# Kernel tuning notes

Measured on AMD Instinct MI355X. Metric: run time of the kernel, lower is better.

The kernel has to match this reference:

```python
import jax, jax.numpy as jnp
import numpy as np

B, T, I, H, O = 256, 128, 64, 2048, 24


def setup_inputs() -> dict:
    key = jax.random.key(0)
    ks = jax.random.split(key, 10)
    sI = 1.0 / np.sqrt(I)
    sH = 1.0 / np.sqrt(H)
    return {
        "trains": jax.random.normal(ks[0], (B, T, I), jnp.float32),
        "dec": jax.random.normal(ks[1], (B, O - 1), jnp.float32),
        # packed gate projections, order [i, f, o, c] along last dim
        "Wx": jax.random.normal(ks[2], (I, 4 * H), jnp.float32) * sI,
        "bx": jax.random.normal(ks[3], (4 * H,), jnp.float32) * sI,
        "Wh": jax.random.normal(ks[4], (H, 4 * H), jnp.float32) * sH,
        "bh": jax.random.normal(ks[5], (4 * H,), jnp.float32) * sH,
        "Win": jax.random.normal(ks[6], (1, I), jnp.float32),
        "b_in": jax.random.normal(ks[7], (I,), jnp.float32),
        "Wout": jax.random.normal(ks[8], (H, 1), jnp.float32) * sH,
        "bout": jax.random.normal(ks[9], (1,), jnp.float32) * sH,
    }


def reference(trains, dec, Wx, bx, Wh, bh, Win, b_in, Wout, bout):
    def cell(h, c, x):
        # fused gate GEMMs: x@Wx and h@Wh each produce all 4 gates at once
        g = x @ Wx + bx + h @ Wh + bh  # [B, 4H]
        i, f, o, cc = jnp.split(g, 4, axis=-1)
        c = jax.nn.sigmoid(f) * c + jax.nn.sigmoid(i) * jnp.tanh(cc)
        h = jax.nn.sigmoid(o) * jnp.tanh(c)
        return h, c

    b = trains.shape[0]
    hdim = Wh.shape[0]
    h0 = jnp.zeros((b, hdim), trains.dtype)
    c0 = jnp.zeros((b, hdim), trains.dtype)

    def enc_step(carry, x):
        h, c = cell(*carry, x)
        return (h, c), None

    (h, c), _ = jax.lax.scan(enc_step, (h0, c0), jnp.swapaxes(trains, 0, 1))
    y1 = h @ Wout + bout  # [B, 1]

    def dec_step(carry, x_scalar):
        x = x_scalar[:, None] @ Win + b_in  # [B, I]
        h, c = cell(*carry, x)
        return (h, c), h @ Wout + bout  # emit [B, 1]

    (h, c), ys = jax.lax.scan(dec_step, (h, c), dec.T)  # ys: [O-1, B, 1]
    return jnp.concatenate([y1, jnp.swapaxes(ys[..., 0], 0, 1)], axis=1)  # [B, O]
```

## Files before the change

### kernel.cpp

```cpp
#include <hip/hip_runtime.h>


#define NB 256
#define NH 2048
#define NI 64
#define NK 2112
#define NPK 8192
#define NSTEPS 151
#define NO 24

typedef int i32x4 __attribute__((ext_vector_type(4)));
typedef int i32x16 __attribute__((ext_vector_type(16)));
typedef float f32x4 __attribute__((ext_vector_type(4)));
typedef unsigned short u16;
typedef unsigned char u8;
typedef unsigned long long u64;

__device__ __forceinline__ void gload16(const void* g, void* l) {
  __builtin_amdgcn_global_load_lds(
      (const __attribute__((address_space(1))) unsigned int*)g,
      (__attribute__((address_space(3))) unsigned int*)l, 16, 0, 0);
}

__device__ __forceinline__ int q8(float v) {
  int q = __float2int_rn(v);
  return q > 127 ? 127 : (q < -127 ? -127 : q);
}

__device__ __forceinline__ float sigmoidf_(float x) { return 1.f / (1.f + __expf(-x)); }
__device__ __forceinline__ float tanhf_(float x) {
  x = fminf(15.f, fmaxf(-15.f, x));
  float e = __expf(2.f * x);
  return (e - 1.f) / (e + 1.f);
}

__global__ __launch_bounds__(256) void wl_colmax(const float* __restrict__ Wx,
                                                 const float* __restrict__ Wh,
                                                 float* __restrict__ sp,
                                                 float* __restrict__ rq) {
  __shared__ float red[4][64];
  const int jl = threadIdx.x & 63, ks = threadIdx.x >> 6;
  const int j = blockIdx.x * 64 + jl;
  float m = 0.f;
  for (int k = ks * 528; k < ks * 528 + 528; ++k) {
    float v = (k < NH) ? Wh[(size_t)k * NPK + j] : Wx[(size_t)(k - NH) * NPK + j];
    m = fmaxf(m, fabsf(v));
  }
  red[ks][jl] = m;
  __syncthreads();
  if (ks == 0) {
    m = fmaxf(fmaxf(red[0][jl], red[1][jl]), fmaxf(red[2][jl], red[3][jl]));
    int p = (j & (NH - 1)) * 4 + (j >> 11);
    sp[p] = m * (1.f / 127.f);
    rq[p] = (m > 0.f) ? 127.f / m : 0.f;
  }
}

__global__ __launch_bounds__(256) void wl_pack_w(const float* __restrict__ Wx,
                                                 const float* __restrict__ Wh,
                                                 const float* __restrict__ rq,
                                                 u8* __restrict__ Wq) {
  __shared__ float s[64][65];
  const int j0 = blockIdx.x * 64, k0 = blockIdx.y * 64;
  const int jl = threadIdx.x & 63, kg = threadIdx.x >> 6;
#pragma unroll
  for (int it = 0; it < 16; ++it) {
    int kl = it * 4 + kg;
    int k = k0 + kl, j = j0 + jl;
    float v = (k < NH) ? Wh[(size_t)k * NPK + j] : Wx[(size_t)(k - NH) * NPK + j];
    s[kl][jl] = v;
  }
  __syncthreads();
  const int j = j0 + jl;
  const int p = (j & (NH - 1)) * 4 + (j >> 11);
  const int cs = p >> 6, col = p & 63;
  const float r = rq[p];
  union { u8 b[16]; i32x4 v; } q;
#pragma unroll
  for (int e = 0; e < 16; ++e) q.b[e] = (u8)(signed char)q8(s[kg * 16 + e][jl] * r);
  *(i32x4*)(Wq + ((size_t)(cs * 33 + blockIdx.y) * 4 + kg) * 1024 + col * 16) = q.v;
}

__global__ __launch_bounds__(256) void wl_bsum(const float* __restrict__ bx,
                                               const float* __restrict__ bh,
                                               float* __restrict__ bsum) {
  int p = blockIdx.x * 256 + threadIdx.x;
  int j = (p & 3) * NH + (p >> 2);
  bsum[p] = bx[j] + bh[j];
}

__global__ __launch_bounds__(256) void wl_xall(const float* __restrict__ trains,
                                               const float* __restrict__ dec,
                                               const float* __restrict__ Win,
                                               const float* __restrict__ b_in,
                                               u8* __restrict__ xfH,
                                               u8* __restrict__ xfL,
                                               float* __restrict__ sx) {
  const int t = blockIdx.x, b = threadIdx.x;
  float x[64];
  if (t < 128) {
    const float4* src = (const float4*)(trains + ((size_t)b * 128 + t) * 64);
#pragma unroll
    for (int i = 0; i < 16; ++i) {
      float4 v = src[i];
      x[4 * i] = v.x; x[4 * i + 1] = v.y; x[4 * i + 2] = v.z; x[4 * i + 3] = v.w;
    }
  } else {
    float d = dec[b * 23 + (t - 128)];
#pragma unroll
    for (int i = 0; i < 64; ++i) x[i] = d * Win[i] + b_in[i];
  }
  float m = 0.f;
#pragma unroll
  for (int i = 0; i < 64; ++i) m = fmaxf(m, fabsf(x[i]));
  float sv, r;
  if (m > 1e-30f) { sv = m * (1.f / 127.f); r = 127.f / m; }
  else            { sv = 1.f; r = 0.f; }
  sx[t * 256 + b] = sv;
  const size_t base = (size_t)t * 16384 + (b >> 5) * 2048;
#pragma unroll
  for (int kc = 0; kc < 2; ++kc)
#pragma unroll
    for (int lhh = 0; lhh < 2; ++lhh) {
      union { u8 b16[16]; i32x4 v; } wh, wl;
#pragma unroll
      for (int e = 0; e < 16; ++e) {
        float xs = x[kc * 32 + lhh * 16 + e] * r;
        int hi = q8(xs);
        int lo = q8((xs - (float)hi) * 254.f);
        wh.b16[e] = (u8)(signed char)hi;
        wl.b16[e] = (u8)(signed char)lo;
      }
      size_t off = base + kc * 1024 + (lhh * 32 + (b & 31)) * 16;
      *(i32x4*)(xfH + off) = wh.v;
      *(i32x4*)(xfL + off) = wl.v;
    }
}

__global__ __launch_bounds__(256, 1) void wl_step(const u8* __restrict__ Wq,
                                                  const float* __restrict__ bsum,
                                                  const float* __restrict__ sp,
                                                  const u8* __restrict__ xfH,
                                                  const u8* __restrict__ xfL,
                                                  const float* __restrict__ sx,
                                                  u8* __restrict__ hfH,
                                                  u8* __restrict__ hfL,
                                                  float* __restrict__ c_t,
                                                  float* __restrict__ ypart,
                                                  const float* __restrict__ Wout,
                                                  int t) {
  __shared__ char arena[90112];

  const int bid = blockIdx.x;
  const int cs = (bid & 7) * 16 + ((bid >> 3) & 15);
  const int rh = bid >> 7;
  const int p0 = cs * 64, u0 = cs * 16, b0 = rh * 128;

  const int tid = threadIdx.x;
  const int wv = tid >> 6, lane = tid & 63;
  const int l31 = lane & 31, lh = lane >> 5;

  const int par = t & 1;
  const u8* __restrict__ hinH = hfH + (size_t)par * 524288;
  const u8* __restrict__ hinL = hfL + (size_t)par * 524288;
  u8* __restrict__ houtH = hfH + (size_t)(par ^ 1) * 524288;
  u8* __restrict__ houtL = hfL + (size_t)(par ^ 1) * 524288;

  const int rb = rh * 4 + wv;
  const size_t aoff = (size_t)rb * 65536 + lane * 16;
  const size_t xoff = (size_t)t * 16384 + rb * 2048 + lane * 16;
  const u8* const wsrc = Wq + (size_t)cs * 135168 + wv * 1024 + lane * 16;

  i32x16 aH0h = {}, aH0l = {}, aH1h = {}, aH1l = {};
  i32x16 aX0h = {}, aX0l = {}, aX1h = {}, aX1l = {};
  i32x4 A[4][4];

  auto stageB = [&](int kt, int buf) {
    gload16(wsrc + (size_t)kt * 4096, arena + buf * 4096 + wv * 1024);
  };
  auto loadA = [&](int kt, int slot) {
    if (kt < 32) {
      A[slot][0] = *(const i32x4*)(hinH + aoff + (size_t)(2 * kt) * 1024);
      A[slot][1] = *(const i32x4*)(hinH + aoff + (size_t)(2 * kt + 1) * 1024);
      A[slot][2] = *(const i32x4*)(hinL + aoff + (size_t)(2 * kt) * 1024);
      A[slot][3] = *(const i32x4*)(hinL + aoff + (size_t)(2 * kt + 1) * 1024);
    } else {
      A[slot][0] = *(const i32x4*)(xfH + xoff);
      A[slot][1] = *(const i32x4*)(xfH + xoff + 1024);
      A[slot][2] = *(const i32x4*)(xfL + xoff);
      A[slot][3] = *(const i32x4*)(xfL + xoff + 1024);
    }
  };
  auto compute = [&](int kt, int buf) {
    const char* Bb = arena + buf * 4096;
    const int slot = kt & 3;
#pragma unroll
    for (int kh = 0; kh < 2; ++kh) {
      i32x4 b0 = *(const i32x4*)(Bb + (kh * 2 + lh) * 1024 + l31 * 16);
      i32x4 b1 = *(const i32x4*)(Bb + (kh * 2 + lh) * 1024 + (32 + l31) * 16);
      i32x4 ah = A[slot][kh], al = A[slot][2 + kh];
      if (kt < 32) {
        aH0h = __builtin_amdgcn_mfma_i32_32x32x32_i8(ah, b0, aH0h, 0, 0, 0);
        aH1h = __builtin_amdgcn_mfma_i32_32x32x32_i8(ah, b1, aH1h, 0, 0, 0);
        aH0l = __builtin_amdgcn_mfma_i32_32x32x32_i8(al, b0, aH0l, 0, 0, 0);
        aH1l = __builtin_amdgcn_mfma_i32_32x32x32_i8(al, b1, aH1l, 0, 0, 0);
      } else {
        aX0h = __builtin_amdgcn_mfma_i32_32x32x32_i8(ah, b0, aX0h, 0, 0, 0);
        aX1h = __builtin_amdgcn_mfma_i32_32x32x32_i8(ah, b1, aX1h, 0, 0, 0);
        aX0l = __builtin_amdgcn_mfma_i32_32x32x32_i8(al, b0, aX0l, 0, 0, 0);
        aX1l = __builtin_amdgcn_mfma_i32_32x32x32_i8(al, b1, aX1l, 0, 0, 0);
      }
    }
  };

  stageB(0, 0); stageB(1, 1); stageB(2, 2); stageB(3, 3);
  loadA(0, 0); loadA(1, 1); loadA(2, 2);
#pragma unroll
  for (int kt = 0; kt < 33; ++kt) {
    if (kt + 4 <= 32) stageB(kt + 4, (kt + 4) % 6);
    if (kt + 3 <= 32) loadA(kt + 3, (kt + 3) & 3);
    if (kt == 0)       asm volatile("s_waitcnt vmcnt(13)" ::: "memory");
    else if (kt == 1)  asm volatile("s_waitcnt vmcnt(14)" ::: "memory");
    else if (kt <= 28) asm volatile("s_waitcnt vmcnt(15)" ::: "memory");
    else if (kt == 29) asm volatile("s_waitcnt vmcnt(14)" ::: "memory");
    else if (kt == 30) asm volatile("s_waitcnt vmcnt(9)" ::: "memory");
    else if (kt == 31) asm volatile("s_waitcnt vmcnt(4)" ::: "memory");
    else               asm volatile("s_waitcnt vmcnt(0)" ::: "memory");
    asm volatile("s_barrier" ::: "memory");
    compute(kt, kt % 6);
  }

  {
    char* const gH = arena + 24576;
    char* const gX = arena + 57344;
    const float s0 = sp[p0 + l31], s1 = sp[p0 + 32 + l31];
#pragma unroll
    for (int cb = 0; cb < 2; ++cb) {
      const i32x16& ahh = cb ? aH1h : aH0h;
      const i32x16& ahl = cb ? aH1l : aH0l;
      const i32x16& axh = cb ? aX1h : aX0h;
      const i32x16& axl = cb ? aX1l : aX0l;
      const float spc = cb ? s1 : s0;
      const float fH = spc * (1.f / 127.f);
      const int col = cb * 32 + l31;
#pragma unroll
      for (int q = 0; q < 4; ++q) {
        f32x4 vH, vX;
#pragma unroll
        for (int e = 0; e < 4; ++e) {
          vH[e] = fH * ((float)ahh[4 * q + e] + (float)ahl[4 * q + e] * (1.f / 254.f));
          vX[e] = spc * ((float)axh[4 * q + e] + (float)axl[4 * q + e] * (1.f / 254.f));
        }
        int chunk = wv * 8 + q * 2 + lh;
        *(f32x4*)(gH + col * 512 + ((chunk ^ (col & 7)) << 4)) = vH;
        *(f32x4*)(gX + col * 512 + ((chunk ^ (col & 7)) << 4)) = vX;
      }
    }
  }
  __syncthreads();

  {
    const char* const gH = arena + 24576;
    const char* const gX = arena + 57344;
    const int bl = tid & 127, ug = tid >> 7;
    const int bg = b0 + bl;
    const float sxv = sx[t * 256 + bg];
    const bool emit = (t >= 127);
    float yacc = 0.f;
    union { u8 q[8]; u64 v; } hqh, hql;
#pragma unroll
    for (int j = 0; j < 8; ++j) {
      int ul = ug * 8 + j;
      float g[4];
#pragma unroll
      for (int gi = 0; gi < 4; ++gi) {
        int col = ul * 4 + gi;
        int off = col * 512 + (((bl >> 2) ^ (col & 7)) << 4) + (bl & 3) * 4;
        g[gi] = *(const float*)(gH + off) + sxv * *(const float*)(gX + off);
      }
      const float4 bs = *(const float4*)(bsum + p0 + ul * 4);
      float si = sigmoidf_(g[0] + bs.x);
      float sf = sigmoidf_(g[1] + bs.y);
      float so = sigmoidf_(g[2] + bs.z);
      float tc = tanhf_(g[3] + bs.w);
      size_t ci = (size_t)(u0 + ul) * NB + bg;
      float cn = sf * c_t[ci] + si * tc;
      float h = so * tanhf_(cn);
      c_t[ci] = cn;
      float hs = h * 127.f;
      int hi = q8(hs);
      int lo = q8((hs - (float)hi) * 254.f);
      hqh.q[j] = (u8)(signed char)hi;
      hql.q[j] = (u8)(signed char)lo;
      if (emit) yacc += h * Wout[u0 + ul];
    }
    size_t hoff = ((size_t)((bg >> 5) * 64 + (cs >> 1)) * 64 +
                   (cs & 1) * 32 + (bg & 31)) * 16 + ug * 8;
    *(u64*)(houtH + hoff) = hqh.v;
    *(u64*)(houtL + hoff) = hql.v;
    if (emit) ypart[((size_t)(t - 127) * 256 + cs * 2 + ug) * NB + bg] = yacc;
  }
}

__global__ __launch_bounds__(256) void wl_finy(const float* __restrict__ ypart,
                                               const float* __restrict__ bout,
                                               float* __restrict__ out) {
  int j = blockIdx.x;
  int b = threadIdx.x;
  const float* yp = ypart + (size_t)j * 256 * NB;
  float s = bout[0];
#pragma unroll 8
  for (int i = 0; i < 256; ++i) s += yp[i * NB + b];
  out[b * NO + j] = s;
}

extern "C" void kernel_launch(void* const* d_in, const int* in_sizes, int n_in,
                              void* d_out, int out_size, void* d_ws, size_t ws_size,
                              hipStream_t stream) {
  const float* trains = (const float*)d_in[0];
  const float* dec    = (const float*)d_in[1];
  const float* Wx     = (const float*)d_in[2];
  const float* bx     = (const float*)d_in[3];
  const float* Wh     = (const float*)d_in[4];
  const float* bh     = (const float*)d_in[5];
  const float* Win    = (const float*)d_in[6];
  const float* b_in   = (const float*)d_in[7];
  const float* Wout   = (const float*)d_in[8];
  const float* bout   = (const float*)d_in[9];
  float* out = (float*)d_out;
  char* ws = (char*)d_ws;

  u8*    Wq    = (u8*)(ws);
  float* sp    = (float*)(ws + 17301504);
  float* rq    = (float*)(ws + 17334272);
  float* bsum  = (float*)(ws + 17367040);
  u8*    xfH   = (u8*)(ws + 17399808);
  u8*    xfL   = (u8*)(ws + 19873792);
  float* sx    = (float*)(ws + 22347776);
  u8*    hfH   = (u8*)(ws + 23550976);
  u8*    hfL   = (u8*)(ws + 24599552);
  float* c_t   = (float*)(ws + 25648128);
  float* ypart = (float*)(ws + 27745280);

  (void)hipMemsetAsync(ws + 23550976, 0, 4194304, stream);
  wl_colmax<<<128, 256, 0, stream>>>(Wx, Wh, sp, rq);
  wl_pack_w<<<dim3(128, 33), 256, 0, stream>>>(Wx, Wh, rq, Wq);
  wl_bsum<<<32, 256, 0, stream>>>(bx, bh, bsum);
  wl_xall<<<NSTEPS, 256, 0, stream>>>(trains, dec, Win, b_in, xfH, xfL, sx);
  for (int t = 0; t < NSTEPS; ++t)
    wl_step<<<256, 256, 0, stream>>>(Wq, bsum, sp, xfH, xfL, sx, hfH, hfL,
                                     c_t, ypart, Wout, t);
  wl_finy<<<NO, 256, 0, stream>>>(ypart, bout, out);
}
```

Before: 2.447 ms.

## Retile LSTM step to 128x64 tiles with LDS-staged A and split colmax

The per-step kernel now gives each block 128 packed gate columns by 64 batch rows instead of 64 columns by 128 rows. Both the h/x operand and the weight tiles are staged through LDS with async global-to-LDS loads in a 6-deep ring, replacing per-wave register prefetch of A. The weight column-max prep is split into a two-stage reduction over 8 k-chunks to expose more parallelism. LDS use rises to 160KB per block and the swizzle and output layouts change to match.

```diff
diff --git a/kernel.cpp b/kernel.cpp
--- a/kernel.cpp
+++ b/kernel.cpp
@@ -34,26 +34,36 @@
   return (e - 1.f) / (e + 1.f);
 }
 
-__global__ __launch_bounds__(256) void wl_colmax(const float* __restrict__ Wx,
-                                                 const float* __restrict__ Wh,
-                                                 float* __restrict__ sp,
-                                                 float* __restrict__ rq) {
+__global__ __launch_bounds__(256) void wl_colmax1(const float* __restrict__ Wx,
+                                                  const float* __restrict__ Wh,
+                                                  float* __restrict__ pmax) {
   __shared__ float red[4][64];
   const int jl = threadIdx.x & 63, ks = threadIdx.x >> 6;
   const int j = blockIdx.x * 64 + jl;
+  const int k0 = blockIdx.y * 264 + ks * 66;
   float m = 0.f;
-  for (int k = ks * 528; k < ks * 528 + 528; ++k) {
+  for (int i = 0; i < 66; ++i) {
+    int k = k0 + i;
     float v = (k < NH) ? Wh[(size_t)k * NPK + j] : Wx[(size_t)(k - NH) * NPK + j];
     m = fmaxf(m, fabsf(v));
   }
   red[ks][jl] = m;
   __syncthreads();
-  if (ks == 0) {
-    m = fmaxf(fmaxf(red[0][jl], red[1][jl]), fmaxf(red[2][jl], red[3][jl]));
-    int p = (j & (NH - 1)) * 4 + (j >> 11);
-    sp[p] = m * (1.f / 127.f);
-    rq[p] = (m > 0.f) ? 127.f / m : 0.f;
-  }
+  if (ks == 0)
+    pmax[(size_t)blockIdx.y * NPK + j] =
+        fmaxf(fmaxf(red[0][jl], red[1][jl]), fmaxf(red[2][jl], red[3][jl]));
+}
+
+__global__ __launch_bounds__(256) void wl_colmax2(const float* __restrict__ pmax,
+                                                  float* __restrict__ sp,
+                                                  float* __restrict__ rq) {
+  int p = blockIdx.x * 256 + threadIdx.x;
+  int j = (p >> 2) | ((p & 3) << 11);
+  float m = 0.f;
+#pragma unroll
+  for (int kb = 0; kb < 8; ++kb) m = fmaxf(m, pmax[(size_t)kb * NPK + j]);
+  sp[p] = m * (1.f / 127.f);
+  rq[p] = (m > 0.f) ? 127.f / m : 0.f;
 }
 
 __global__ __launch_bounds__(256) void wl_pack_w(const float* __restrict__ Wx,
@@ -73,12 +83,12 @@
   __syncthreads();
   const int j = j0 + jl;
   const int p = (j & (NH - 1)) * 4 + (j >> 11);
-  const int cs = p >> 6, col = p & 63;
+  const int csq = p >> 6, col = p & 63;
   const float r = rq[p];
   union { u8 b[16]; i32x4 v; } q;
 #pragma unroll
   for (int e = 0; e < 16; ++e) q.b[e] = (u8)(signed char)q8(s[kg * 16 + e][jl] * r);
-  *(i32x4*)(Wq + ((size_t)(cs * 33 + blockIdx.y) * 4 + kg) * 1024 + col * 16) = q.v;
+  *(i32x4*)(Wq + ((size_t)(csq * 33 + blockIdx.y) * 4 + kg) * 1024 + col * 16) = q.v;
 }
 
 __global__ __launch_bounds__(256) void wl_bsum(const float* __restrict__ bx,
@@ -149,12 +159,13 @@
                                                   float* __restrict__ ypart,
                                                   const float* __restrict__ Wout,
                                                   int t) {
-  __shared__ char arena[90112];
+  __shared__ char arena[163840];
 
   const int bid = blockIdx.x;
-  const int cs = (bid & 7) * 16 + ((bid >> 3) & 15);
-  const int rh = bid >> 7;
-  const int p0 = cs * 64, u0 = cs * 16, b0 = rh * 128;
+  const int cs = (bid & 7) * 8 + ((bid >> 3) & 7);
+  const int rh = bid >> 6;
+  const int p0 = cs * 128, u0 = cs * 32, b0 = rh * 64;
+  const int rbg = rh * 2;
 
   const int tid = threadIdx.x;
   const int wv = tid >> 6, lane = tid & 63;
@@ -166,64 +177,61 @@
   u8* __restrict__ houtH = hfH + (size_t)(par ^ 1) * 524288;
   u8* __restrict__ houtL = hfL + (size_t)(par ^ 1) * 524288;
 
-  const int rb = rh * 4 + wv;
-  const size_t aoff = (size_t)rb * 65536 + lane * 16;
-  const size_t xoff = (size_t)t * 16384 + rb * 2048 + lane * 16;
-  const u8* const wsrc = Wq + (size_t)cs * 135168 + wv * 1024 + lane * 16;
-
-  i32x16 aH0h = {}, aH0l = {}, aH1h = {}, aH1l = {};
-  i32x16 aX0h = {}, aX0l = {}, aX1h = {}, aX1l = {};
-  i32x4 A[4][4];
-
-  auto stageB = [&](int kt, int buf) {
-    gload16(wsrc + (size_t)kt * 4096, arena + buf * 4096 + wv * 1024);
+  i32x16 aHh[2] = {}, aHl[2] = {}, aXh[2] = {}, aXl[2] = {};
+
+  auto stage = [&](int kt, int buf) {
+    char* const base = arena + buf * 16384;
+#pragma unroll
+    for (int i = 0; i < 4; ++i) {
+      int c = wv * 4 + i;
+      const u8* src;
+      char* dst;
+      if (c < 8) {
+        int s = c >> 2, rb = (c >> 1) & 1, hl = c & 1;
+        const u8* hb = hl ? hinL : hinH;
+        const u8* xb = hl ? xfL : xfH;
+        src = (kt < 32)
+                  ? hb + ((size_t)(rbg + rb) * 64 + 2 * kt + s) * 1024
+                  : xb + (size_t)t * 16384 + (rbg + rb) * 2048 + s * 1024;
+        dst = base + c * 1024;
+      } else {
+        int cb = (c >> 2) & 1, kg = c & 3;
+        src = Wq + ((size_t)((cs * 2 + cb) * 33 + kt) * 4 + kg) * 1024;
+        dst = base + 8192 + ((cb << 2) + kg) * 1024;
+      }
+      gload16(src + lane * 16, dst);
+    }
   };
-  auto loadA = [&](int kt, int slot) {
-    if (kt < 32) {
-      A[slot][0] = *(const i32x4*)(hinH + aoff + (size_t)(2 * kt) * 1024);
-      A[slot][1] = *(const i32x4*)(hinH + aoff + (size_t)(2 * kt + 1) * 1024);
-      A[slot][2] = *(const i32x4*)(hinL + aoff + (size_t)(2 * kt) * 1024);
-      A[slot][3] = *(const i32x4*)(hinL + aoff + (size_t)(2 * kt + 1) * 1024);
-    } else {
-      A[slot][0] = *(const i32x4*)(xfH + xoff);
-      A[slot][1] = *(const i32x4*)(xfH + xoff + 1024);
-      A[slot][2] = *(const i32x4*)(xfL + xoff);
-      A[slot][3] = *(const i32x4*)(xfL + xoff + 1024);
+
+  auto compute = [&](int kt, int buf) {
+    const char* Ab = arena + buf * 16384;
+    const char* Bb = Ab + 8192;
+    const int cb = wv >> 1, cl = (wv & 1) * 32 + l31;
+#pragma unroll
+    for (int s = 0; s < 2; ++s) {
+      i32x4 bf = *(const i32x4*)(Bb + ((cb << 2) + (s << 1) + lh) * 1024 + cl * 16);
+#pragma unroll
+      for (int m = 0; m < 2; ++m) {
+        i32x4 ah = *(const i32x4*)(Ab + (s * 4 + m * 2 + 0) * 1024 + lane * 16);
+        i32x4 al = *(const i32x4*)(Ab + (s * 4 + m * 2 + 1) * 1024 + lane * 16);
+        if (kt < 32) {
+          aHh[m] = __builtin_amdgcn_mfma_i32_32x32x32_i8(ah, bf, aHh[m], 0, 0, 0);
+          aHl[m] = __builtin_amdgcn_mfma_i32_32x32x32_i8(al, bf, aHl[m], 0, 0, 0);
+        } else {
+          aXh[m] = __builtin_amdgcn_mfma_i32_32x32x32_i8(ah, bf, aXh[m], 0, 0, 0);
+          aXl[m] = __builtin_amdgcn_mfma_i32_32x32x32_i8(al, bf, aXl[m], 0, 0, 0);
+        }
+      }
     }
   };
-  auto compute = [&](int kt, int buf) {
-    const char* Bb = arena + buf * 4096;
-    const int slot = kt & 3;
-#pragma unroll
-    for (int kh = 0; kh < 2; ++kh) {
-      i32x4 b0 = *(const i32x4*)(Bb + (kh * 2 + lh) * 1024 + l31 * 16);
-      i32x4 b1 = *(const i32x4*)(Bb + (kh * 2 + lh) * 1024 + (32 + l31) * 16);
-      i32x4 ah = A[slot][kh], al = A[slot][2 + kh];
-      if (kt < 32) {
-        aH0h = __builtin_amdgcn_mfma_i32_32x32x32_i8(ah, b0, aH0h, 0, 0, 0);
-        aH1h = __builtin_amdgcn_mfma_i32_32x32x32_i8(ah, b1, aH1h, 0, 0, 0);
-        aH0l = __builtin_amdgcn_mfma_i32_32x32x32_i8(al, b0, aH0l, 0, 0, 0);
-        aH1l = __builtin_amdgcn_mfma_i32_32x32x32_i8(al, b1, aH1l, 0, 0, 0);
-      } else {
-        aX0h = __builtin_amdgcn_mfma_i32_32x32x32_i8(ah, b0, aX0h, 0, 0, 0);
-        aX1h = __builtin_amdgcn_mfma_i32_32x32x32_i8(ah, b1, aX1h, 0, 0, 0);
-        aX0l = __builtin_amdgcn_mfma_i32_32x32x32_i8(al, b0, aX0l, 0, 0, 0);
-        aX1l = __builtin_amdgcn_mfma_i32_32x32x32_i8(al, b1, aX1l, 0, 0, 0);
-      }
-    }
-  };
-
-  stageB(0, 0); stageB(1, 1); stageB(2, 2); stageB(3, 3);
-  loadA(0, 0); loadA(1, 1); loadA(2, 2);
+
+  stage(0, 0); stage(1, 1); stage(2, 2); stage(3, 3);
 #pragma unroll
   for (int kt = 0; kt < 33; ++kt) {
-    if (kt + 4 <= 32) stageB(kt + 4, (kt + 4) % 6);
-    if (kt + 3 <= 32) loadA(kt + 3, (kt + 3) & 3);
-    if (kt == 0)       asm volatile("s_waitcnt vmcnt(13)" ::: "memory");
-    else if (kt == 1)  asm volatile("s_waitcnt vmcnt(14)" ::: "memory");
-    else if (kt <= 28) asm volatile("s_waitcnt vmcnt(15)" ::: "memory");
-    else if (kt == 29) asm volatile("s_waitcnt vmcnt(14)" ::: "memory");
-    else if (kt == 30) asm volatile("s_waitcnt vmcnt(9)" ::: "memory");
+    if (kt + 4 <= 32) stage(kt + 4, (kt + 4) % 6);
+    if (kt <= 28)      asm volatile("s_waitcnt vmcnt(16)" ::: "memory");
+    else if (kt == 29) asm volatile("s_waitcnt vmcnt(12)" ::: "memory");
+    else if (kt == 30) asm volatile("s_waitcnt vmcnt(8)" ::: "memory");
     else if (kt == 31) asm volatile("s_waitcnt vmcnt(4)" ::: "memory");
     else               asm volatile("s_waitcnt vmcnt(0)" ::: "memory");
     asm volatile("s_barrier" ::: "memory");
@@ -231,38 +239,32 @@
   }
 
   {
-    char* const gH = arena + 24576;
-    char* const gX = arena + 57344;
-    const float s0 = sp[p0 + l31], s1 = sp[p0 + 32 + l31];
-#pragma unroll
-    for (int cb = 0; cb < 2; ++cb) {
-      const i32x16& ahh = cb ? aH1h : aH0h;
-      const i32x16& ahl = cb ? aH1l : aH0l;
-      const i32x16& axh = cb ? aX1h : aX0h;
-      const i32x16& axl = cb ? aX1l : aX0l;
-      const float spc = cb ? s1 : s0;
-      const float fH = spc * (1.f / 127.f);
-      const int col = cb * 32 + l31;
+    char* const gH = arena + 98304;
+    char* const gX = arena + 131072;
+    const int col = wv * 32 + l31;
+    const float spc = sp[p0 + col];
+    const float fH = spc * (1.f / 127.f);
+#pragma unroll
+    for (int m = 0; m < 2; ++m)
 #pragma unroll
       for (int q = 0; q < 4; ++q) {
         f32x4 vH, vX;
 #pragma unroll
         for (int e = 0; e < 4; ++e) {
-          vH[e] = fH * ((float)ahh[4 * q + e] + (float)ahl[4 * q + e] * (1.f / 254.f));
-          vX[e] = spc * ((float)axh[4 * q + e] + (float)axl[4 * q + e] * (1.f / 254.f));
+          vH[e] = fH * ((float)aHh[m][4 * q + e] + (float)aHl[m][4 * q + e] * (1.f / 254.f));
+          vX[e] = spc * ((float)aXh[m][4 * q + e] + (float)aXl[m][4 * q + e] * (1.f / 254.f));
         }
-        int chunk = wv * 8 + q * 2 + lh;
-        *(f32x4*)(gH + col * 512 + ((chunk ^ (col & 7)) << 4)) = vH;
-        *(f32x4*)(gX + col * 512 + ((chunk ^ (col & 7)) << 4)) = vX;
-      }
-    }
+        int chunk = m * 8 + q * 2 + lh;
+        *(f32x4*)(gH + col * 256 + ((chunk ^ (col & 15)) << 4)) = vH;
+        *(f32x4*)(gX + col * 256 + ((chunk ^ (col & 15)) << 4)) = vX;
+      }
   }
   __syncthreads();
 
   {
-    const char* const gH = arena + 24576;
-    const char* const gX = arena + 57344;
-    const int bl = tid & 127, ug = tid >> 7;
+    const char* const gH = arena + 98304;
+    const char* const gX = arena + 131072;
+    const int bl = tid & 63, ug = tid >> 6;
     const int bg = b0 + bl;
     const float sxv = sx[t * 256 + bg];
     const bool emit = (t >= 127);
@@ -275,7 +277,7 @@
 #pragma unroll
       for (int gi = 0; gi < 4; ++gi) {
         int col = ul * 4 + gi;
-        int off = col * 512 + (((bl >> 2) ^ (col & 7)) << 4) + (bl & 3) * 4;
+        int off = col * 256 + (((bl >> 2) ^ (col & 15)) << 4) + (bl & 3) * 4;
         g[gi] = *(const float*)(gH + off) + sxv * *(const float*)(gX + off);
       }
       const float4 bs = *(const float4*)(bsum + p0 + ul * 4);
@@ -294,11 +296,11 @@
       hql.q[j] = (u8)(signed char)lo;
       if (emit) yacc += h * Wout[u0 + ul];
     }
-    size_t hoff = ((size_t)((bg >> 5) * 64 + (cs >> 1)) * 64 +
-                   (cs & 1) * 32 + (bg & 31)) * 16 + ug * 8;
+    size_t hoff = ((size_t)((bg >> 5) * 64 + cs) * 64 +
+                   (ug >> 1) * 32 + (bg & 31)) * 16 + (ug & 1) * 8;
     *(u64*)(houtH + hoff) = hqh.v;
     *(u64*)(houtL + hoff) = hql.v;
-    if (emit) ypart[((size_t)(t - 127) * 256 + cs * 2 + ug) * NB + bg] = yacc;
+    if (emit) ypart[((size_t)(t - 127) * 256 + cs * 4 + ug) * NB + bg] = yacc;
   }
 }
 
@@ -341,9 +343,11 @@
   u8*    hfL   = (u8*)(ws + 24599552);
   float* c_t   = (float*)(ws + 25648128);
   float* ypart = (float*)(ws + 27745280);
+  float* pmax  = (float*)(ws + 34036736);
 
   (void)hipMemsetAsync(ws + 23550976, 0, 4194304, stream);
-  wl_colmax<<<128, 256, 0, stream>>>(Wx, Wh, sp, rq);
+  wl_colmax1<<<dim3(128, 8), 256, 0, stream>>>(Wx, Wh, pmax);
+  wl_colmax2<<<32, 256, 0, stream>>>(pmax, sp, rq);
   wl_pack_w<<<dim3(128, 33), 256, 0, stream>>>(Wx, Wh, rq, Wq);
   wl_bsum<<<32, 256, 0, stream>>>(bx, bh, bsum);
   wl_xall<<<NSTEPS, 256, 0, stream>>>(trains, dec, Win, b_in, xfH, xfL, sx);
```

After: 3.027 ms. +23.7%, slower.
